# Kernel tuning notes

Measured on AMD Instinct MI355X. Metric: run time of the kernel, lower is better.

The kernel has to match this reference:

```python
import jax, jax.numpy as jnp
import numpy as np

DEPTH, DIM, HEADS, HD, CTX, B = 4, 768, 12, 64, 2048, 4
INNER = HEADS * HD  # 768
EPS = 1e-5  # torch LayerNorm default


def _ln(x, g, b):
    m = jnp.mean(x, axis=-1, keepdims=True)
    v = jnp.var(x, axis=-1, keepdims=True)
    return (x - m) * jax.lax.rsqrt(v + EPS) * g + b


def setup_inputs() -> dict:
    key = jax.random.key(0)
    ks = jax.random.split(key, 12)
    s = 0.02
    return {
        "x": jax.random.normal(ks[0], (B, CTX, DIM), dtype=jnp.float32),
        "pos_emb": jax.random.normal(ks[1], (1, CTX, DIM), dtype=jnp.float32),
        # per-layer params stacked on leading depth axis
        "ln1_g": jnp.ones((DEPTH, DIM), jnp.float32),
        "ln1_b": jnp.zeros((DEPTH, DIM), jnp.float32),
        "Wq": jax.random.normal(ks[2], (DEPTH, DIM, INNER), dtype=jnp.float32) * s,
        "Wk": jax.random.normal(ks[3], (DEPTH, DIM, INNER), dtype=jnp.float32) * s,
        "Wv": jax.random.normal(ks[4], (DEPTH, DIM, INNER), dtype=jnp.float32) * s,
        "Wo": jax.random.normal(ks[5], (DEPTH, INNER, DIM), dtype=jnp.float32) * s,
        "ln2_g": jnp.ones((DEPTH, DIM), jnp.float32),
        "ln2_b": jnp.zeros((DEPTH, DIM), jnp.float32),
        "W1": jax.random.normal(ks[6], (DEPTH, DIM, DIM), dtype=jnp.float32) * s,  # hidden_dim == dim per source
        "b1": jnp.zeros((DEPTH, DIM), jnp.float32),
        "W2": jax.random.normal(ks[7], (DEPTH, DIM, DIM), dtype=jnp.float32) * s,
        "b2": jnp.zeros((DEPTH, DIM), jnp.float32),
    }


def reference(x, pos_emb, ln1_g, ln1_b, Wq, Wk, Wv, Wo, ln2_g, ln2_b, W1, b1, W2, b2):
    scale = 1.0 / np.sqrt(HD).astype(np.float32)
    x = x + pos_emb
    b, n, _ = x.shape
    for i in range(DEPTH):
        # --- attention block (pre-LN, residual) ---
        h = _ln(x, ln1_g[i], ln1_b[i])
        q = (h @ Wq[i]).reshape(b, n, HEADS, HD)
        k = (h @ Wk[i]).reshape(b, n, HEADS, HD)
        v = (h @ Wv[i]).reshape(b, n, HEADS, HD)
        scores = jnp.einsum('bihd,bjhd->bhij', q, k) * scale
        attn = jax.nn.softmax(scores, axis=-1)
        o = jnp.einsum('bhij,bjhd->bihd', attn, v).reshape(b, n, INNER)
        x = x + o @ Wo[i]
        # --- feed-forward block (LN -> Linear -> GELU -> Linear, residual) ---
        h = _ln(x, ln2_g[i], ln2_b[i])
        h = jax.nn.gelu(h @ W1[i] + b1[i], approximate=False)
        x = x + (h @ W2[i] + b2[i])
    return x
```

## Files before the change

kernel.cpp:

```cpp
#include <hip/hip_runtime.h>
#include <math.h>


#define DEPTH 4
#define DIM   768
#define HEADS 12
#define HD    64
#define CTXN  2048
#define BATCH 4
#define TOKENS (BATCH * CTXN)
#define QKVS  (3 * DIM)

typedef unsigned short u16;
typedef short s16x8 __attribute__((ext_vector_type(8)));
typedef float f32x4 __attribute__((ext_vector_type(4)));
typedef u16  u16x4 __attribute__((ext_vector_type(4)));

__device__ __forceinline__ u16 f2bf(float f) {
  union { float f; unsigned u; } c;
  c.f = f;
  unsigned u = c.u;
  return (u16)((u + 0x7FFFu + ((u >> 16) & 1u)) >> 16);
}

__device__ __forceinline__ s16x8 ldfrag(const u16* t, int r, int g) {
  return *(const s16x8*)(t + r * 64 + 8 * (g ^ (r & 7)));
}
__device__ __forceinline__ void stfrag(u16* t, int r, int g, s16x8 v) {
  *(s16x8*)(t + r * 64 + 8 * (g ^ (r & 7))) = v;
}

__device__ __forceinline__ void gld_lds16(const u16* g, u16* l) {
#if __has_builtin(__builtin_amdgcn_global_load_lds)
  __builtin_amdgcn_global_load_lds(
      (const __attribute__((address_space(1))) unsigned int*)g,
      (__attribute__((address_space(3))) unsigned int*)l, 16, 0, 0);
#else
  int lane = threadIdx.x & 63;
  *(s16x8*)(l + lane * 8) = *(const s16x8*)(g);
#endif
}

__global__ __launch_bounds__(256) void add_pos_kernel(
    const float* __restrict__ X, const float* __restrict__ P,
    float* __restrict__ Y, int n, int pn) {
  int i = blockIdx.x * 256 + threadIdx.x;
  if (i < n) Y[i] = X[i] + P[i % pn];
}

__global__ __launch_bounds__(256) void wconv_kernel(
    const float* __restrict__ Wq, const float* __restrict__ Wk,
    const float* __restrict__ Wv, const float* __restrict__ Wo,
    const float* __restrict__ W1, const float* __restrict__ W2,
    u16* __restrict__ dst) {
  int mat = blockIdx.z;
  int layer = mat / 6, type = mat % 6;
  const float* srcs[6] = {Wq, Wk, Wv, Wo, W1, W2};
  const float* src = srcs[type] + (size_t)layer * DIM * DIM;
  u16* d = dst + (size_t)mat * DIM * DIM;
  __shared__ float L[32][33];
  int k0 = blockIdx.y * 32, n0 = blockIdx.x * 32;
  int r = threadIdx.x >> 3, c4 = (threadIdx.x & 7) * 4;
  float4 v = *(const float4*)&src[(size_t)(k0 + r) * DIM + n0 + c4];
  L[c4 + 0][r] = v.x; L[c4 + 1][r] = v.y;
  L[c4 + 2][r] = v.z; L[c4 + 3][r] = v.w;
  __syncthreads();
  u16x4 w;
#pragma unroll
  for (int j = 0; j < 4; ++j) w[j] = f2bf(L[r][c4 + j]);
  *(u16x4*)&d[(size_t)(n0 + r) * DIM + k0 + c4] = w;
}

__global__ __launch_bounds__(256) void ln_kernel(
    const float* __restrict__ X, const float* __restrict__ g,
    const float* __restrict__ b, u16* __restrict__ Y) {
  int t = blockIdx.x;
  int tid = threadIdx.x;
  const float* xr = X + (size_t)t * DIM;
  float v0 = xr[tid], v1 = xr[tid + 256], v2 = xr[tid + 512];
  float s = v0 + v1 + v2;
  float q = v0 * v0 + v1 * v1 + v2 * v2;
#pragma unroll
  for (int o = 32; o > 0; o >>= 1) {
    s += __shfl_xor(s, o);
    q += __shfl_xor(q, o);
  }
  __shared__ float rs[4], rq[4];
  int w = tid >> 6;
  if ((tid & 63) == 0) { rs[w] = s; rq[w] = q; }
  __syncthreads();
  s = rs[0] + rs[1] + rs[2] + rs[3];
  q = rq[0] + rq[1] + rq[2] + rq[3];
  float mean = s * (1.0f / DIM);
  float var  = q * (1.0f / DIM) - mean * mean;
  float r = rsqrtf(var + 1e-5f);
  u16* yr = Y + (size_t)t * DIM;
  yr[tid]       = f2bf((v0 - mean) * r * g[tid]       + b[tid]);
  yr[tid + 256] = f2bf((v1 - mean) * r * g[tid + 256] + b[tid + 256]);
  yr[tid + 512] = f2bf((v2 - mean) * r * g[tid + 512] + b[tid + 512]);
}

template <int HAS_BIAS, int HAS_GELU, int HAS_RES, int OUT_BF16>
__global__ __launch_bounds__(256, 3) void gemm_bf16(
    const u16* __restrict__ A, const u16* __restrict__ Bt,
    const float* __restrict__ bias, void* __restrict__ Cv, int Nc) {
  float* C = (float*)Cv;
  u16* Cb = (u16*)Cv;
  __shared__ __align__(16) u16 As[128 * 64];
  __shared__ __align__(16) u16 Bs[128 * 64];
  int tid = threadIdx.x;
  int wave = tid >> 6, lane = tid & 63, ln = lane & 15, quad = lane >> 4;
  int wr = wave >> 1, wc = wave & 1;
  int m0 = blockIdx.y * 128, n0 = blockIdx.x * 128;

  int srow = wave * 32 + (lane >> 3);
  int sg = (lane & 7) ^ ((lane >> 3) & 7);
  const u16* ga = A + (size_t)(m0 + srow) * DIM + sg * 8;
  const u16* gb = Bt + (size_t)(n0 + srow) * DIM + sg * 8;
  u16* la = As + wave * 2048;
  u16* lb = Bs + wave * 2048;

  f32x4 acc[4][4];
  const f32x4 zero = {0.0f, 0.0f, 0.0f, 0.0f};
#pragma unroll
  for (int i = 0; i < 4; ++i)
#pragma unroll
    for (int j = 0; j < 4; ++j) acc[i][j] = zero;

  for (int kt = 0; kt < DIM / 64; ++kt) {
#pragma unroll
    for (int i = 0; i < 4; ++i) {
      gld_lds16(ga + (size_t)i * 8 * DIM, la + i * 512);
      gld_lds16(gb + (size_t)i * 8 * DIM, lb + i * 512);
    }
    ga += 64; gb += 64;
    __syncthreads();

    s16x8 bfr0[4], bfr1[4];
#pragma unroll
    for (int ni = 0; ni < 4; ++ni) {
      bfr0[ni] = ldfrag(Bs, wc * 64 + ni * 16 + ln, quad);
      bfr1[ni] = ldfrag(Bs, wc * 64 + ni * 16 + ln, 4 + quad);
    }
#pragma unroll
    for (int mi = 0; mi < 4; ++mi) {
      s16x8 a0 = ldfrag(As, wr * 64 + mi * 16 + ln, quad);
      s16x8 a1 = ldfrag(As, wr * 64 + mi * 16 + ln, 4 + quad);
#pragma unroll
      for (int ni = 0; ni < 4; ++ni) {
        acc[mi][ni] = __builtin_amdgcn_mfma_f32_16x16x32_bf16(a0, bfr0[ni], acc[mi][ni], 0, 0, 0);
        acc[mi][ni] = __builtin_amdgcn_mfma_f32_16x16x32_bf16(a1, bfr1[ni], acc[mi][ni], 0, 0, 0);
      }
    }
    __syncthreads();
  }

#pragma unroll
  for (int ni = 0; ni < 4; ++ni) {
    int c = n0 + wc * 64 + ni * 16 + ln;
    float bv = HAS_BIAS ? bias[c] : 0.0f;
#pragma unroll
    for (int mi = 0; mi < 4; ++mi) {
#pragma unroll
      for (int reg = 0; reg < 4; ++reg) {
        int r = m0 + wr * 64 + mi * 16 + quad * 4 + reg;
        float v = acc[mi][ni][reg] + bv;
        if (HAS_GELU) v = 0.5f * v * (1.0f + erff(v * 0.70710678118654752f));
        size_t o = (size_t)r * Nc + c;
        if (OUT_BF16) { Cb[o] = f2bf(v); }
        else if (HAS_RES) { C[o] += v; }
        else { C[o] = v; }
      }
    }
  }
}

__global__ __launch_bounds__(256) void vtrans_kernel(
    const u16* __restrict__ QKV, u16* __restrict__ Vt) {
  int bid = blockIdx.x;
  int tt = bid & 31;
  int h  = (bid >> 5) % HEADS;
  int b  = bid / (32 * HEADS);
  int tid = threadIdx.x;
  __shared__ u16 T[64][66];
  const u16* src = QKV + ((size_t)(b * CTXN + tt * 64)) * QKVS + 2 * DIM + h * HD;
#pragma unroll
  for (int i = 0; i < 2; ++i) {
    int idx = tid + i * 256, r = idx >> 3, g = idx & 7;
    s16x8 v = *(const s16x8*)&src[(size_t)r * QKVS + g * 8];
#pragma unroll
    for (int j = 0; j < 8; ++j) T[g * 8 + j][r] = (u16)v[j];
  }
  __syncthreads();
#pragma unroll
  for (int i = 0; i < 2; ++i) {
    int idx = tid + i * 256, d = idx >> 3, g = idx & 7;
    s16x8 w;
#pragma unroll
    for (int j = 0; j < 8; ++j) w[j] = (short)T[d][g * 8 + j];
    *(s16x8*)&Vt[((size_t)(b * HEADS + h) * HD + d) * CTXN + tt * 64 + g * 8] = w;
  }
}

__global__ __launch_bounds__(256) void attn_kernel(
    const u16* __restrict__ QKV, const u16* __restrict__ Vt,
    u16* __restrict__ Ob) {
  const int tiles = CTXN / 64;
  int bid = blockIdx.x;
  int qt = bid % tiles;
  int h  = (bid / tiles) % HEADS;
  int b  = bid / (tiles * HEADS);
  int tid = threadIdx.x;
  int wave = tid >> 6, lane = tid & 63, ln = lane & 15, quad = lane >> 4;

  __shared__ __align__(16) char smem[24576];
  u16* Ks = (u16*)smem;
  u16* Vs = (u16*)(smem + 8192);
  u16* Ps = (u16*)(smem + 16384);
  float (*Of)[65] = (float (*)[65])smem;

  const u16* qrow =
      QKV + ((size_t)(b * CTXN + qt * 64 + wave * 16 + ln)) * QKVS + h * HD;
  s16x8 aq0 = *(const s16x8*)&qrow[quad * 8];
  s16x8 aq1 = *(const s16x8*)&qrow[32 + quad * 8];

  float m = -1e30f, l = 0.0f;
  f32x4 oacc[4];
  const f32x4 zero = {0.0f, 0.0f, 0.0f, 0.0f};
#pragma unroll
  for (int i = 0; i < 4; ++i) oacc[i] = zero;

  const u16* kb0 = QKV + ((size_t)b * CTXN) * QKVS + DIM + h * HD;
  const u16* vt0 = Vt + ((size_t)(b * HEADS + h) * HD) * CTXN;
  const float lg = 0.125f * 1.4426950408889634f;
  const float THR = 44.3614195f;

  int sr0 = tid >> 3, sg0 = tid & 7;
  int sr1 = sr0 + 32;
  const u16* kp0 = kb0 + (size_t)sr0 * QKVS + sg0 * 8;
  const u16* kp1 = kb0 + (size_t)sr1 * QKVS + sg0 * 8;
  const u16* vp0 = vt0 + (size_t)sr0 * CTXN + sg0 * 8;
  const u16* vp1 = vt0 + (size_t)sr1 * CTXN + sg0 * 8;

  s16x8 rk0 = *(const s16x8*)kp0;
  s16x8 rk1 = *(const s16x8*)kp1;
  s16x8 rv0 = *(const s16x8*)vp0;
  s16x8 rv1 = *(const s16x8*)vp1;

  for (int kt = 0; kt < tiles; ++kt) {
    stfrag(Ks, sr0, sg0, rk0);
    stfrag(Ks, sr1, sg0, rk1);
    stfrag(Vs, sr0, sg0, rv0);
    stfrag(Vs, sr1, sg0, rv1);
    __syncthreads();

    {
      int ktn = (kt + 1 < tiles) ? kt + 1 : kt;
      rk0 = *(const s16x8*)(kp0 + (size_t)ktn * 64 * QKVS);
      rk1 = *(const s16x8*)(kp1 + (size_t)ktn * 64 * QKVS);
      rv0 = *(const s16x8*)(vp0 + (size_t)ktn * 64);
      rv1 = *(const s16x8*)(vp1 + (size_t)ktn * 64);
    }

    f32x4 sacc[4];
#pragma unroll
    for (int nb = 0; nb < 4; ++nb) {
      sacc[nb] = zero;
      s16x8 k0 = ldfrag(Ks, nb * 16 + ln, quad);
      s16x8 k1 = ldfrag(Ks, nb * 16 + ln, 4 + quad);
      sacc[nb] = __builtin_amdgcn_mfma_f32_16x16x32_bf16(k0, aq0, sacc[nb], 0, 0, 0);
      sacc[nb] = __builtin_amdgcn_mfma_f32_16x16x32_bf16(k1, aq1, sacc[nb], 0, 0, 0);
    }

    float mx = fmaxf(fmaxf(sacc[0][0], sacc[0][1]), fmaxf(sacc[0][2], sacc[0][3]));
#pragma unroll
    for (int nb = 1; nb < 4; ++nb)
      mx = fmaxf(mx, fmaxf(fmaxf(sacc[nb][0], sacc[nb][1]),
                           fmaxf(sacc[nb][2], sacc[nb][3])));
    mx = fmaxf(mx, __shfl_xor(mx, 16));
    mx = fmaxf(mx, __shfl_xor(mx, 32));

    if (!__all(mx <= m + THR)) {
      float mnew = fmaxf(m, mx);
      float alpha = exp2f((m - mnew) * lg);
      float ar[4];
#pragma unroll
      for (int reg = 0; reg < 4; ++reg) ar[reg] = __shfl(alpha, quad * 4 + reg);
#pragma unroll
      for (int nb = 0; nb < 4; ++nb)
#pragma unroll
        for (int reg = 0; reg < 4; ++reg) oacc[nb][reg] *= ar[reg];
      l *= alpha;
      m = mnew;
    }

    float nm = -m * lg;
    float ls = 0.0f;
    u16x4 pk[4];
#pragma unroll
    for (int nb = 0; nb < 4; ++nb) {
#pragma unroll
      for (int reg = 0; reg < 4; ++reg) {
        float p = exp2f(fmaf(sacc[nb][reg], lg, nm));
        ls += p;
        pk[nb][reg] = f2bf(p);
      }
    }
    ls += __shfl_xor(ls, 16);
    ls += __shfl_xor(ls, 32);
    l += ls;

    {
      int row = wave * 16 + ln;
      int rs = row & 7;
      int half = (quad & 1) * 4;
#pragma unroll
      for (int nb = 0; nb < 4; ++nb) {
        int g0 = nb * 2 + (quad >> 1);
        *(u16x4*)&Ps[row * 64 + 8 * (g0 ^ rs) + half] = pk[nb];
      }
    }
    __syncthreads();

    s16x8 ap0 = ldfrag(Ps, wave * 16 + ln, quad);
    s16x8 ap1 = ldfrag(Ps, wave * 16 + ln, 4 + quad);
#pragma unroll
    for (int nb = 0; nb < 4; ++nb) {
      s16x8 bv0 = ldfrag(Vs, nb * 16 + ln, quad);
      s16x8 bv1 = ldfrag(Vs, nb * 16 + ln, 4 + quad);
      oacc[nb] = __builtin_amdgcn_mfma_f32_16x16x32_bf16(ap0, bv0, oacc[nb], 0, 0, 0);
      oacc[nb] = __builtin_amdgcn_mfma_f32_16x16x32_bf16(ap1, bv1, oacc[nb], 0, 0, 0);
    }
    __syncthreads();
  }

  float li[4];
#pragma unroll
  for (int reg = 0; reg < 4; ++reg) li[reg] = 1.0f / __shfl(l, quad * 4 + reg);

#pragma unroll
  for (int nb = 0; nb < 4; ++nb)
#pragma unroll
    for (int reg = 0; reg < 4; ++reg)
      Of[wave * 16 + quad * 4 + reg][nb * 16 + ln] = oacc[nb][reg] * li[reg];
  __syncthreads();
  {
    int r = tid >> 2, c0 = (tid & 3) * 16;
    u16* dst = Ob + ((size_t)(b * CTXN + qt * 64 + r)) * DIM + h * HD + c0;
#pragma unroll
    for (int k = 0; k < 4; ++k) {
      u16x4 w;
#pragma unroll
      for (int j = 0; j < 4; ++j) w[j] = f2bf(Of[r][c0 + 4 * k + j]);
      *(u16x4*)&dst[4 * k] = w;
    }
  }
}

extern "C" void kernel_launch(void* const* d_in, const int* in_sizes, int n_in,
                              void* d_out, int out_size, void* d_ws, size_t ws_size,
                              hipStream_t stream) {
  const float* x_in  = (const float*)d_in[0];
  const float* pos   = (const float*)d_in[1];
  const float* ln1_g = (const float*)d_in[2];
  const float* ln1_b = (const float*)d_in[3];
  const float* Wq    = (const float*)d_in[4];
  const float* Wk    = (const float*)d_in[5];
  const float* Wv    = (const float*)d_in[6];
  const float* Wo    = (const float*)d_in[7];
  const float* ln2_g = (const float*)d_in[8];
  const float* ln2_b = (const float*)d_in[9];
  const float* W1    = (const float*)d_in[10];
  const float* b1    = (const float*)d_in[11];
  const float* W2    = (const float*)d_in[12];
  const float* b2    = (const float*)d_in[13];

  float* x = (float*)d_out;
  const size_t TD = (size_t)TOKENS * DIM;
  u16* hb  = (u16*)d_ws;
  u16* qkv = hb + TD;
  u16* vt  = qkv + 3 * TD;
  u16* wt  = vt + TD;
  u16* fb  = qkv;

  int n = (int)TD, pn = CTXN * DIM;
  add_pos_kernel<<<(n + 255) / 256, 256, 0, stream>>>(x_in, pos, x, n, pn);
  {
    dim3 wg(24, 24, 24);
    wconv_kernel<<<wg, 256, 0, stream>>>(Wq, Wk, Wv, Wo, W1, W2, wt);
  }

  const size_t WSZ = (size_t)DIM * DIM;
  dim3 gq(QKVS / 128, TOKENS / 128);
  dim3 gg(DIM / 128, TOKENS / 128);
  int nblk_attn = BATCH * HEADS * (CTXN / 64);
  for (int i = 0; i < DEPTH; ++i) {
    const u16* wqkv = wt + (size_t)(i * 6 + 0) * WSZ;
    const u16* wo   = wt + (size_t)(i * 6 + 3) * WSZ;
    const u16* w1   = wt + (size_t)(i * 6 + 4) * WSZ;
    const u16* w2   = wt + (size_t)(i * 6 + 5) * WSZ;

    ln_kernel<<<TOKENS, 256, 0, stream>>>(x, ln1_g + i * DIM, ln1_b + i * DIM, hb);
    gemm_bf16<0,0,0,1><<<gq, 256, 0, stream>>>(hb, wqkv, nullptr, qkv, QKVS);
    vtrans_kernel<<<nblk_attn, 256, 0, stream>>>(qkv, vt);
    attn_kernel<<<nblk_attn, 256, 0, stream>>>(qkv, vt, hb);
    gemm_bf16<0,0,1,0><<<gg, 256, 0, stream>>>(hb, wo, nullptr, x, DIM);

    ln_kernel<<<TOKENS, 256, 0, stream>>>(x, ln2_g + i * DIM, ln2_b + i * DIM, hb);
    gemm_bf16<1,1,0,1><<<gg, 256, 0, stream>>>(hb, w1, b1 + i * DIM, fb, DIM);
    gemm_bf16<1,0,1,0><<<gg, 256, 0, stream>>>(fb, w2, b2 + i * DIM, x, DIM);
  }
}
```

Before: 1.228 ms.

## Shrink N=768 GEMM tiles, swizzle workgroup order, prioritize attention MFMA

The GEMM gets a templated M-tile, and the three N=768 GEMMs use 64-row tiles, doubling their grid to 768 blocks for better CU fill. GEMM and attention blocks are remapped with an XCD-style swizzle so neighbouring tiles share L2. The attention kernel raises wave priority around its MFMA sections and uses a cheaper round-half-up bf16 conversion for probabilities. The smaller tiles lower per-block arithmetic intensity, and the fast conversion changes rounding slightly.

```diff
diff --git a/kernel.cpp b/kernel.cpp
--- a/kernel.cpp
+++ b/kernel.cpp
@@ -21,6 +21,12 @@
   c.f = f;
   unsigned u = c.u;
   return (u16)((u + 0x7FFFu + ((u >> 16) & 1u)) >> 16);
+}
+
+__device__ __forceinline__ u16 f2bf_fast(float f) {
+  union { float f; unsigned u; } c;
+  c.f = f;
+  return (u16)((c.u + 0x8000u) >> 16);
 }
 
 __device__ __forceinline__ s16x8 ldfrag(const u16* t, int r, int g) {
@@ -100,39 +106,47 @@
   yr[tid + 512] = f2bf((v2 - mean) * r * g[tid + 512] + b[tid + 512]);
 }
 
-template <int HAS_BIAS, int HAS_GELU, int HAS_RES, int OUT_BF16>
+template <int BM, int HAS_BIAS, int HAS_GELU, int HAS_RES, int OUT_BF16>
 __global__ __launch_bounds__(256, 3) void gemm_bf16(
     const u16* __restrict__ A, const u16* __restrict__ Bt,
     const float* __restrict__ bias, void* __restrict__ Cv, int Nc) {
+  constexpr int MI = BM / 32;
   float* C = (float*)Cv;
   u16* Cb = (u16*)Cv;
-  __shared__ __align__(16) u16 As[128 * 64];
+  __shared__ __align__(16) u16 As[BM * 64];
   __shared__ __align__(16) u16 Bs[128 * 64];
   int tid = threadIdx.x;
   int wave = tid >> 6, lane = tid & 63, ln = lane & 15, quad = lane >> 4;
   int wr = wave >> 1, wc = wave & 1;
-  int m0 = blockIdx.y * 128, n0 = blockIdx.x * 128;
-
-  int srow = wave * 32 + (lane >> 3);
+
+  int nwg = gridDim.x * gridDim.y;
+  int lin = blockIdx.y * gridDim.x + blockIdx.x;
+  int swz = (lin & 7) * (nwg >> 3) + (lin >> 3);
+  int bx = swz % gridDim.x, by = swz / gridDim.x;
+  int m0 = by * BM, n0 = bx * 128;
+
   int sg = (lane & 7) ^ ((lane >> 3) & 7);
-  const u16* ga = A + (size_t)(m0 + srow) * DIM + sg * 8;
-  const u16* gb = Bt + (size_t)(n0 + srow) * DIM + sg * 8;
-  u16* la = As + wave * 2048;
+  int srowA = wave * (BM / 4) + (lane >> 3);
+  int srowB = wave * 32 + (lane >> 3);
+  const u16* ga = A + (size_t)(m0 + srowA) * DIM + sg * 8;
+  const u16* gb = Bt + (size_t)(n0 + srowB) * DIM + sg * 8;
+  u16* la = As + wave * (BM / 4) * 64;
   u16* lb = Bs + wave * 2048;
 
-  f32x4 acc[4][4];
+  f32x4 acc[MI][4];
   const f32x4 zero = {0.0f, 0.0f, 0.0f, 0.0f};
 #pragma unroll
-  for (int i = 0; i < 4; ++i)
+  for (int i = 0; i < MI; ++i)
 #pragma unroll
     for (int j = 0; j < 4; ++j) acc[i][j] = zero;
 
   for (int kt = 0; kt < DIM / 64; ++kt) {
 #pragma unroll
-    for (int i = 0; i < 4; ++i) {
+    for (int i = 0; i < MI; ++i)
       gld_lds16(ga + (size_t)i * 8 * DIM, la + i * 512);
+#pragma unroll
+    for (int i = 0; i < 4; ++i)
       gld_lds16(gb + (size_t)i * 8 * DIM, lb + i * 512);
-    }
     ga += 64; gb += 64;
     __syncthreads();
 
@@ -143,9 +157,9 @@
       bfr1[ni] = ldfrag(Bs, wc * 64 + ni * 16 + ln, 4 + quad);
     }
 #pragma unroll
-    for (int mi = 0; mi < 4; ++mi) {
-      s16x8 a0 = ldfrag(As, wr * 64 + mi * 16 + ln, quad);
-      s16x8 a1 = ldfrag(As, wr * 64 + mi * 16 + ln, 4 + quad);
+    for (int mi = 0; mi < MI; ++mi) {
+      s16x8 a0 = ldfrag(As, wr * (BM / 2) + mi * 16 + ln, quad);
+      s16x8 a1 = ldfrag(As, wr * (BM / 2) + mi * 16 + ln, 4 + quad);
 #pragma unroll
       for (int ni = 0; ni < 4; ++ni) {
         acc[mi][ni] = __builtin_amdgcn_mfma_f32_16x16x32_bf16(a0, bfr0[ni], acc[mi][ni], 0, 0, 0);
@@ -160,10 +174,10 @@
     int c = n0 + wc * 64 + ni * 16 + ln;
     float bv = HAS_BIAS ? bias[c] : 0.0f;
 #pragma unroll
-    for (int mi = 0; mi < 4; ++mi) {
+    for (int mi = 0; mi < MI; ++mi) {
 #pragma unroll
       for (int reg = 0; reg < 4; ++reg) {
-        int r = m0 + wr * 64 + mi * 16 + quad * 4 + reg;
+        int r = m0 + wr * (BM / 2) + mi * 16 + quad * 4 + reg;
         float v = acc[mi][ni][reg] + bv;
         if (HAS_GELU) v = 0.5f * v * (1.0f + erff(v * 0.70710678118654752f));
         size_t o = (size_t)r * Nc + c;
@@ -206,7 +220,9 @@
     const u16* __restrict__ QKV, const u16* __restrict__ Vt,
     u16* __restrict__ Ob) {
   const int tiles = CTXN / 64;
-  int bid = blockIdx.x;
+  const int nblk = BATCH * HEADS * tiles;
+  int orig = blockIdx.x;
+  int bid = (orig & 7) * (nblk >> 3) + (orig >> 3);
   int qt = bid % tiles;
   int h  = (bid / tiles) % HEADS;
   int b  = bid / (tiles * HEADS);
@@ -263,6 +279,7 @@
     }
 
     f32x4 sacc[4];
+    __builtin_amdgcn_s_setprio(1);
 #pragma unroll
     for (int nb = 0; nb < 4; ++nb) {
       sacc[nb] = zero;
@@ -271,6 +288,7 @@
       sacc[nb] = __builtin_amdgcn_mfma_f32_16x16x32_bf16(k0, aq0, sacc[nb], 0, 0, 0);
       sacc[nb] = __builtin_amdgcn_mfma_f32_16x16x32_bf16(k1, aq1, sacc[nb], 0, 0, 0);
     }
+    __builtin_amdgcn_s_setprio(0);
 
     float mx = fmaxf(fmaxf(sacc[0][0], sacc[0][1]), fmaxf(sacc[0][2], sacc[0][3]));
 #pragma unroll
@@ -303,7 +321,7 @@
       for (int reg = 0; reg < 4; ++reg) {
         float p = exp2f(fmaf(sacc[nb][reg], lg, nm));
         ls += p;
-        pk[nb][reg] = f2bf(p);
+        pk[nb][reg] = f2bf_fast(p);
       }
     }
     ls += __shfl_xor(ls, 16);
@@ -324,6 +342,7 @@
 
     s16x8 ap0 = ldfrag(Ps, wave * 16 + ln, quad);
     s16x8 ap1 = ldfrag(Ps, wave * 16 + ln, 4 + quad);
+    __builtin_amdgcn_s_setprio(1);
 #pragma unroll
     for (int nb = 0; nb < 4; ++nb) {
       s16x8 bv0 = ldfrag(Vs, nb * 16 + ln, quad);
@@ -331,6 +350,7 @@
       oacc[nb] = __builtin_amdgcn_mfma_f32_16x16x32_bf16(ap0, bv0, oacc[nb], 0, 0, 0);
       oacc[nb] = __builtin_amdgcn_mfma_f32_16x16x32_bf16(ap1, bv1, oacc[nb], 0, 0, 0);
     }
+    __builtin_amdgcn_s_setprio(0);
     __syncthreads();
   }
 
@@ -392,7 +412,7 @@
 
   const size_t WSZ = (size_t)DIM * DIM;
   dim3 gq(QKVS / 128, TOKENS / 128);
-  dim3 gg(DIM / 128, TOKENS / 128);
+  dim3 gg(DIM / 128, TOKENS / 64);
   int nblk_attn = BATCH * HEADS * (CTXN / 64);
   for (int i = 0; i < DEPTH; ++i) {
     const u16* wqkv = wt + (size_t)(i * 6 + 0) * WSZ;
@@ -401,13 +421,13 @@
     const u16* w2   = wt + (size_t)(i * 6 + 5) * WSZ;
 
     ln_kernel<<<TOKENS, 256, 0, stream>>>(x, ln1_g + i * DIM, ln1_b + i * DIM, hb);
-    gemm_bf16<0,0,0,1><<<gq, 256, 0, stream>>>(hb, wqkv, nullptr, qkv, QKVS);
+    gemm_bf16<128,0,0,0,1><<<gq, 256, 0, stream>>>(hb, wqkv, nullptr, qkv, QKVS);
     vtrans_kernel<<<nblk_attn, 256, 0, stream>>>(qkv, vt);
     attn_kernel<<<nblk_attn, 256, 0, stream>>>(qkv, vt, hb);
-    gemm_bf16<0,0,1,0><<<gg, 256, 0, stream>>>(hb, wo, nullptr, x, DIM);
+    gemm_bf16<64,0,0,1,0><<<gg, 256, 0, stream>>>(hb, wo, nullptr, x, DIM);
 
     ln_kernel<<<TOKENS, 256, 0, stream>>>(x, ln2_g + i * DIM, ln2_b + i * DIM, hb);
-    gemm_bf16<1,1,0,1><<<gg, 256, 0, stream>>>(hb, w1, b1 + i * DIM, fb, DIM);
-    gemm_bf16<1,0,1,0><<<gg, 256, 0, stream>>>(fb, w2, b2 + i * DIM, x, DIM);
-  }
-}
+    gemm_bf16<64,1,1,0,1><<<gg, 256, 0, stream>>>(hb, w1, b1 + i * DIM, fb, DIM);
+    gemm_bf16<64,1,0,1,0><<<gg, 256, 0, stream>>>(fb, w2, b2 + i * DIM, x, DIM);
+  }
+}
```

Result: faster. 1.041 ms (-15.2%).
